# Optimization experiments

Measured on AMD Instinct MI355X. Metric: run time of the kernel, lower is better.

Reference implementation:

```python
import jax, jax.numpy as jnp
import numpy as np
from jax import lax

IMG = 512            # image H = W
FH = FW = 32         # feature map spatial size
A = 9                # anchors per location (3 sizes x 3 ratios)
N = FH * FW * A      # total anchors = 9216
IOU_THR = 0.7
MIN_SCORE = 0.5
MIN_SIZE = 1e-3


def make_anchors():
    """Anchors in centroid format (cx, cy, w, h), ordered (H, W, A)."""
    stride = IMG / FH
    sizes = np.array([32.0, 64.0, 128.0])
    ratios = np.array([0.5, 1.0, 2.0])
    ws = (sizes[:, None] / np.sqrt(ratios)[None, :]).reshape(-1)  # (A,)
    hs = (sizes[:, None] * np.sqrt(ratios)[None, :]).reshape(-1)  # (A,)
    cx = (np.arange(FW) + 0.5) * stride
    cy = (np.arange(FH) + 0.5) * stride
    CX = np.broadcast_to(cx[None, :, None], (FH, FW, A))
    CY = np.broadcast_to(cy[:, None, None], (FH, FW, A))
    Wg = np.broadcast_to(ws[None, None, :], (FH, FW, A))
    Hg = np.broadcast_to(hs[None, None, :], (FH, FW, A))
    anc = np.stack([CX, CY, Wg, Hg], axis=-1).reshape(-1, 4)
    return jnp.asarray(anc, dtype=jnp.float32)


def pairwise_iou(b):
    # b: (N,4) corners x1,y1,x2,y2
    x1, y1, x2, y2 = b[:, 0], b[:, 1], b[:, 2], b[:, 3]
    area = (x2 - x1) * (y2 - y1)
    ix1 = jnp.maximum(x1[:, None], x1[None, :])
    iy1 = jnp.maximum(y1[:, None], y1[None, :])
    ix2 = jnp.minimum(x2[:, None], x2[None, :])
    iy2 = jnp.minimum(y2[:, None], y2[None, :])
    inter = jnp.maximum(ix2 - ix1, 0.0) * jnp.maximum(iy2 - iy1, 0.0)
    union = area[:, None] + area[None, :] - inter
    return inter / jnp.maximum(union, 1e-9)


def nms_keep(boxes, scores, valid):
    """Greedy NMS. Returns bool keep mask of shape (N,). Index decisions only."""
    s = jnp.where(valid, scores, -jnp.inf)
    order = jnp.argsort(-s)
    b = boxes[order]
    v = valid[order]
    ious = pairwise_iou(b)  # (N, N)
    idx = jnp.arange(N)

    def body(i, supp):
        keep_i = (~supp[i]) & v[i]
        return supp | (keep_i & (ious[i] > IOU_THR) & (idx > i))

    supp = lax.fori_loop(0, N, body, jnp.zeros(N, dtype=bool))
    keep_sorted = (~supp) & v
    return jnp.zeros(N, dtype=bool).at[order].set(keep_sorted)


def setup_inputs() -> dict:
    key = jax.random.key(0)
    ks = jax.random.split(key, 4)
    return {
        "feature_map": jax.random.normal(ks[0], (1, 256, FH, FW), jnp.float32),
        "conv1_w": jax.random.normal(ks[1], (512, 256, 3, 3), jnp.float32) * 0.02,
        "conv1_b": jnp.zeros((512,), jnp.float32),
        "conv2_w": jax.random.normal(ks[2], (A, 512), jnp.float32) * 0.01,
        "conv2_b": jnp.zeros((A,), jnp.float32),
        "conv3_w": jax.random.normal(ks[3], (4 * A, 512), jnp.float32) * 0.01,
        "conv3_b": jnp.zeros((4 * A,), jnp.float32),
    }


def reference(feature_map, conv1_w, conv1_b, conv2_w, conv2_b, conv3_w, conv3_b):
    anchors = make_anchors()  # (N,4) cx,cy,w,h

    # --- conv backbone head ---
    h = lax.conv_general_dilated(
        feature_map, conv1_w, (1, 1), "SAME",
        dimension_numbers=("NCHW", "OIHW", "NCHW"))
    h = jax.nn.relu(h + conv1_b[None, :, None, None])  # (1,512,H,W)

    scores = jax.nn.sigmoid(
        jnp.einsum("bchw,ac->bahw", h, conv2_w) + conv2_b[None, :, None, None])
    scores = scores.transpose(0, 2, 3, 1).reshape(-1)  # (N,) ordered (H,W,A)

    off = jnp.einsum("bchw,oc->bohw", h, conv3_w) + conv3_b[None, :, None, None]
    off = off.reshape(1, A, 4, FH, FW).transpose(0, 3, 4, 1, 2).reshape(-1, 4)

    acx, acy, aw, ah = anchors[:, 0], anchors[:, 1], anchors[:, 2], anchors[:, 3]
    cx = acx + off[:, 0] * aw
    cy = acy + off[:, 1] * ah
    bw = aw * jnp.exp(off[:, 2])
    bh = ah * jnp.exp(off[:, 3])
    boxes = jnp.stack([cx - bw / 2, cy - bh / 2, cx + bw / 2, cy + bh / 2], axis=1)

    # --- clip to image ---
    lo = jnp.array([0.0, 0.0, 0.0, 0.0], jnp.float32)
    hi = jnp.array([IMG, IMG, IMG, IMG], jnp.float32)
    boxes = jnp.clip(boxes, lo, hi)

    # --- remove small boxes + score threshold (as a mask, jit-safe) ---
    valid = ((boxes[:, 2] - boxes[:, 0]) >= MIN_SIZE) \
          & ((boxes[:, 3] - boxes[:, 1]) >= MIN_SIZE) \
          & (scores >= MIN_SCORE)

    # --- NMS (selection is index-based; no gradient through the decision) ---
    keep = nms_keep(lax.stop_gradient(boxes), lax.stop_gradient(scores), valid)

    out = jnp.concatenate(
        [boxes * keep[:, None].astype(boxes.dtype),
         (scores * keep.astype(scores.dtype))[:, None]], axis=1)  # (N,5)
    return out
```

## Files before the change

### kernel.cpp

```cpp
#include <hip/hip_runtime.h>
#include <math.h>

#define FHW   32
#define NA    9
#define NBOX  9216
#define C1    256
#define C2    512
#define KTOT  2304
#define KS    8
#define KCH   (KTOT / KS)
#define BK    16
#define NT    (KCH / BK)
#define CAP   64
#define CAPL  4

struct AnchorWH { float w[NA]; float h[NA]; };

#define FP_OFF    0u
#define WT_OFF    1183744u
#define HP_OFF    5902336u
#define BOX_OFF   22679552u
#define SC_OFF    22827008u
#define VL_OFF    22863872u
#define DEG_OFF   22900736u
#define ADJ_OFF   22937600u
#define NV_OFF    24117248u

__global__ __launch_bounds__(256) void k_prep(const float* __restrict__ fin,
                                              float* __restrict__ Fp,
                                              unsigned int* __restrict__ deg,
                                              unsigned int* __restrict__ nv,
                                              const float* __restrict__ w1,
                                              float* __restrict__ Wt,
                                              float* __restrict__ out) {
    if (blockIdx.x < 1156) {
        int idx = blockIdx.x * 256 + threadIdx.x;
        if (idx < 256 * 34 * 34) {
            int c   = idx / 1156;
            int rem = idx - c * 1156;
            int yy  = rem / 34;
            int xx  = rem - yy * 34;
            float v = 0.f;
            if (yy >= 1 && yy <= 32 && xx >= 1 && xx <= 32)
                v = fin[c * 1024 + (yy - 1) * 32 + (xx - 1)];
            Fp[idx] = v;
        }
        if (idx < NBOX)     deg[idx] = 0u;
        if (idx < NBOX * 5) out[idx] = 0.f;
        if (idx == 0)       *nv = 0u;
    } else {
        __shared__ float tile[32][33];
        int tb  = blockIdx.x - 1156;
        int k0  = (tb % 72) * 32;
        int oc0 = (tb / 72) * 32;
        int t   = threadIdx.x;
        int r0 = t >> 5, c = t & 31;
        #pragma unroll
        for (int i = 0; i < 4; ++i) {
            int r = r0 + 8 * i;
            tile[r][c] = w1[(oc0 + r) * KTOT + k0 + c];
        }
        __syncthreads();
        #pragma unroll
        for (int i = 0; i < 4; ++i) {
            int kk  = r0 + 8 * i;
            int k   = k0 + kk;
            int ch  = k / 9;
            int kap = k - ch * 9;
            Wt[(kap * 256 + ch) * C2 + oc0 + c] = tile[c][kk];
        }
    }
}

__global__ __launch_bounds__(256) void k_gemm(const float* __restrict__ Fp,
                                              const float* __restrict__ Wt,
                                              float* __restrict__ hp) {
    const int id = blockIdx.x;
    const int kz = id & 7;
    const int g  = id >> 3;
    const int by = g & 3, bx = g >> 2;
    const int p0  = bx * 128;
    const int oc0 = by * 128;
    const int k0b = kz * KCH;
    const int t  = threadIdx.x;
    const int ty = t >> 4, tx = t & 15;

    __shared__ float As[BK][128];
    __shared__ float Bs[BK][128];

    const int pp  = t & 127;
    const int th  = t >> 7;
    const int pyx = ((p0 + pp) >> 5) * 34 + ((p0 + pp) & 31);
    const int rB  = t >> 5;
    const int cB  = (t & 31) * 4;

    float acc[2][2][4][4];
    #pragma unroll
    for (int rh = 0; rh < 2; ++rh)
        #pragma unroll
        for (int ch = 0; ch < 2; ++ch)
            #pragma unroll
            for (int r = 0; r < 4; ++r)
                #pragma unroll
                for (int c = 0; c < 4; ++c) acc[rh][ch][r][c] = 0.f;

    float  aS[8];
    float4 bS0, bS1;

    auto LOAD = [&](int s) {
        int tap = s >> 8, c0 = s & 255;
        int dy  = (tap * 11) >> 5;
        int dx  = tap - 3 * dy;
        const float* ab = Fp + ((c0 + th) * 34 + dy) * 34 + dx + pyx;
        #pragma unroll
        for (int i = 0; i < 8; ++i) aS[i] = ab[i * 2312];
        const float* bb = Wt + (s + rB) * C2 + oc0 + cB;
        bS0 = *(const float4*)bb;
        bS1 = *(const float4*)(bb + 8 * C2);
    };
    auto STORE = [&]() {
        #pragma unroll
        for (int i = 0; i < 8; ++i) As[2 * i + th][pp] = aS[i];
        *(float4*)&Bs[rB][cB]     = bS0;
        *(float4*)&Bs[rB + 8][cB] = bS1;
    };

    LOAD(k0b);
    #pragma unroll 1
    for (int tile = 0; tile < NT; ++tile) {
        __syncthreads();
        STORE();
        __syncthreads();
        if (tile + 1 < NT) LOAD(k0b + (tile + 1) * BK);
        #pragma unroll
        for (int kk = 0; kk < BK; ++kk) {
            float a[2][4], b[2][4];
            *(float4*)&a[0][0] = *(const float4*)&As[kk][ty * 4];
            *(float4*)&a[1][0] = *(const float4*)&As[kk][ty * 4 + 64];
            *(float4*)&b[0][0] = *(const float4*)&Bs[kk][tx * 4];
            *(float4*)&b[1][0] = *(const float4*)&Bs[kk][tx * 4 + 64];
            #pragma unroll
            for (int rh = 0; rh < 2; ++rh)
                #pragma unroll
                for (int ch = 0; ch < 2; ++ch)
                    #pragma unroll
                    for (int r = 0; r < 4; ++r)
                        #pragma unroll
                        for (int c = 0; c < 4; ++c)
                            acc[rh][ch][r][c] = fmaf(a[rh][r], b[ch][c], acc[rh][ch][r][c]);
        }
    }

    #pragma unroll
    for (int rh = 0; rh < 2; ++rh)
        #pragma unroll
        for (int r = 0; r < 4; ++r) {
            int p = p0 + rh * 64 + ty * 4 + r;
            float* dst = hp + ((size_t)(kz * 1024 + p)) * C2 + oc0 + tx * 4;
            *(float4*)dst        = *(float4*)&acc[rh][0][r][0];
            *(float4*)(dst + 64) = *(float4*)&acc[rh][1][r][0];
        }
}

__global__ __launch_bounds__(256) void k_heads(const float* __restrict__ hp,
                                               const float* __restrict__ b1,
                                               const float* __restrict__ w2,
                                               const float* __restrict__ b2,
                                               const float* __restrict__ w3,
                                               const float* __restrict__ b3,
                                               float* __restrict__ boxes,
                                               float* __restrict__ scoresG,
                                               unsigned int* __restrict__ nv,
                                               unsigned int* __restrict__ vlist,
                                               AnchorWH awh) {
    const int p0 = blockIdx.x * 4;
    const int t  = threadIdx.x;
    __shared__ float hrow[4][C2];
    __shared__ float arr[4][45];

    #pragma unroll
    for (int px = 0; px < 4; ++px) {
        int p = p0 + px;
        #pragma unroll
        for (int i = 0; i < 2; ++i) {
            int c = t + 256 * i;
            float s = b1[c];
            #pragma unroll
            for (int ks = 0; ks < KS; ++ks) s += hp[((size_t)(ks * 1024 + p)) * C2 + c];
            hrow[px][c] = fmaxf(s, 0.f);
        }
    }
    __syncthreads();

    const int w = t >> 6, lane = t & 63;
    for (int job = w; job < 180; job += 4) {
        int px = job / 45, j = job - px * 45;
        const float* wp = (j < 9) ? (w2 + j * C2) : (w3 + (j - 9) * C2);
        float s = 0.f;
        #pragma unroll
        for (int i = 0; i < 8; ++i) s += hrow[px][lane + 64 * i] * wp[lane + 64 * i];
        #pragma unroll
        for (int d = 1; d < 64; d <<= 1) s += __shfl_xor(s, d, 64);
        if (lane == 0) arr[px][j] = s;
    }
    __syncthreads();

    if (t < 36) {
        int px = t / 9, a = t - px * 9;
        int p = p0 + px;
        float logit = arr[px][a] + b2[a];
        float score = 1.f / (1.f + expf(-logit));
        float o0 = arr[px][9 + a * 4 + 0] + b3[a * 4 + 0];
        float o1 = arr[px][9 + a * 4 + 1] + b3[a * 4 + 1];
        float o2 = arr[px][9 + a * 4 + 2] + b3[a * 4 + 2];
        float o3 = arr[px][9 + a * 4 + 3] + b3[a * 4 + 3];
        int y = p >> 5, x = p & 31;
        float ax = (x + 0.5f) * 16.f, ay = (y + 0.5f) * 16.f;
        float aw = awh.w[a], ah = awh.h[a];
        float cx = ax + o0 * aw;
        float cy = ay + o1 * ah;
        float bw = aw * expf(o2);
        float bh = ah * expf(o3);
        float x1 = fminf(fmaxf(cx - bw * 0.5f, 0.f), 512.f);
        float y1 = fminf(fmaxf(cy - bh * 0.5f, 0.f), 512.f);
        float x2 = fminf(fmaxf(cx + bw * 0.5f, 0.f), 512.f);
        float y2 = fminf(fmaxf(cy + bh * 0.5f, 0.f), 512.f);
        int n = p * 9 + a;
        float4 bx4; bx4.x = x1; bx4.y = y1; bx4.z = x2; bx4.w = y2;
        ((float4*)boxes)[n] = bx4;
        scoresG[n] = score;
        bool valid = (x2 - x1 >= 0.001f) && (y2 - y1 >= 0.001f) && (score >= 0.5f);
        if (valid) {
            unsigned int ci = atomicAdd(nv, 1u);
            vlist[ci] = (unsigned int)n;
        }
    }
}

__global__ __launch_bounds__(256) void k_adj(const unsigned int* __restrict__ nvp,
                                             const unsigned int* __restrict__ vlist,
                                             const float* __restrict__ boxes,
                                             const float* __restrict__ scoresG,
                                             unsigned int* __restrict__ deg,
                                             unsigned short* __restrict__ adj) {
    const int Nv = (int)*nvp;
    int b = blockIdx.x;
    int tv = (int)(sqrtf(2.f * b + 0.25f) - 0.5f);
    while ((tv + 1) * (tv + 2) / 2 <= b) tv++;
    while (tv * (tv + 1) / 2 > b) tv--;
    int tu = b - tv * (tv + 1) / 2;
    if (tv * 128 >= Nv) return;

    __shared__ float4 ub[128], vb[128];
    __shared__ float  us[128], vs[128];
    __shared__ int    uo[128], vo[128];
    int t = threadIdx.x;
    if (t < 128) {
        int gi = tu * 128 + t;
        if (gi < Nv) { int n = (int)vlist[gi]; ub[t] = ((const float4*)boxes)[n]; us[t] = scoresG[n]; uo[t] = n; }
        else us[t] = -1.f;
    } else {
        int tt = t - 128;
        int gj = tv * 128 + tt;
        if (gj < Nv) { int n = (int)vlist[gj]; vb[tt] = ((const float4*)boxes)[n]; vs[tt] = scoresG[n]; vo[tt] = n; }
        else vs[tt] = -1.f;
    }
    __syncthreads();

    for (int s = 0; s < 64; ++s) {
        int q  = t + 256 * s;
        int i  = q >> 7, jj = q & 127;
        if (tu == tv && i >= jj) continue;
        float su = us[i], sv = vs[jj];
        if (su < 0.f || sv < 0.f) continue;
        float4 bu = ub[i], bv = vb[jj];
        float au = (bu.z - bu.x) * (bu.w - bu.y);
        float av = (bv.z - bv.x) * (bv.w - bv.y);
        float ix1 = fmaxf(bu.x, bv.x), iy1 = fmaxf(bu.y, bv.y);
        float ix2 = fminf(bu.z, bv.z), iy2 = fminf(bu.w, bv.w);
        float inter = fmaxf(ix2 - ix1, 0.f) * fmaxf(iy2 - iy1, 0.f);
        float uni = au + av - inter;
        float iou = inter / fmaxf(uni, 1e-9f);
        if (iou > 0.7f) {
            int gi = tu * 128 + i, gj = tv * 128 + jj;
            bool uHigh = (su > sv) || (su == sv && uo[i] < vo[jj]);
            int hi = uHigh ? gi : gj;
            int lo = uHigh ? gj : gi;
            unsigned int old = atomicAdd(&deg[hi], 1u);
            if ((old & 0xFFFFu) < CAP) {
                adj[hi * CAP + (old & 0xFFFFu)] = (unsigned short)lo;
                atomicAdd(&deg[lo], 0x10000u);
            }
        }
    }
}

__global__ __launch_bounds__(512) void k_peel(const unsigned int* __restrict__ nvp,
                                              const unsigned int* __restrict__ vlist,
                                              const unsigned int* __restrict__ degG,
                                              const unsigned short* __restrict__ adjG,
                                              const float* __restrict__ boxes,
                                              const float* __restrict__ scoresG,
                                              float* __restrict__ out) {
    __shared__ unsigned int   word[NBOX];
    __shared__ unsigned char  st[NBOX];
    __shared__ unsigned short outL[NBOX * CAPL];
    const int t  = threadIdx.x;
    const int Nv = (int)*nvp;
    const int chunk = (Nv + 511) / 512;
    const int i0 = t * chunk;
    const int i1 = (i0 + chunk < Nv) ? (i0 + chunk) : Nv;

    unsigned int amask = 0, smask = 0;
    for (int i = i0; i < i1; ++i) {
        unsigned int dg = degG[i];
        int cin  = (int)(dg >> 16);
        int dout = (int)(dg & 0xFFFFu); if (dout > CAP) dout = CAP;
        int dl = (dout < CAPL) ? dout : CAPL;
        for (int s = 0; s < dl; ++s)
            outL[i * CAPL + s] = adjG[i * CAP + s];
        word[i] = (unsigned int)cin;
        st[i] = 0;
        if (cin == 0) smask |= 1u << (i - i0);
        else          amask |= 1u << (i - i0);
    }
    __syncthreads();

    auto PUSH = [&](int i, bool kept) {
        unsigned int dg = degG[i];
        int dout = (int)(dg & 0xFFFFu); if (dout > CAP) dout = CAP;
        unsigned int delta = kept ? 0xFFFFu : 0xFFFFFFFFu;
        for (int s = 0; s < dout; ++s) {
            int j = (s < CAPL) ? (int)outL[i * CAPL + s]
                               : (int)adjG[i * CAP + s];
            atomicAdd(&word[j], delta);
        }
    };

    {
        unsigned int m = smask;
        while (m) {
            int b = __ffs(m) - 1; m &= m - 1;
            int i = i0 + b;
            st[i] = 1;
            PUSH(i, true);
        }
    }

    {
        volatile unsigned int* vw = word;
        int idle = 0;
        while (__any(amask != 0u)) {
            bool prog = false;
            unsigned int m = amask;
            while (m) {
                int b = __ffs(m) - 1; m &= m - 1;
                int i = i0 + b;
                unsigned int w = vw[i];
                if ((w & 0xFFFFu) == 0u) {
                    bool kept = (w >> 16) == 0u;
                    st[i] = kept ? 1 : 2;
                    PUSH(i, kept);
                    amask &= ~(1u << b);
                    prog = true;
                }
            }
            if (__any(prog)) idle = 0;
            else {
                if (++idle > 8000) break;
                __builtin_amdgcn_s_sleep(1);
            }
        }
    }
    __syncthreads();

    for (int i = i0; i < i1; ++i) {
        if (st[i] == 1) {
            int n = (int)vlist[i];
            float4 b = ((const float4*)boxes)[n];
            out[n * 5 + 0] = b.x;
            out[n * 5 + 1] = b.y;
            out[n * 5 + 2] = b.z;
            out[n * 5 + 3] = b.w;
            out[n * 5 + 4] = scoresG[n];
        }
    }
}

extern "C" void kernel_launch(void* const* d_in, const int* in_sizes, int n_in,
                              void* d_out, int out_size, void* d_ws, size_t ws_size,
                              hipStream_t stream) {
    const float* fin = (const float*)d_in[0];
    const float* w1  = (const float*)d_in[1];
    const float* b1  = (const float*)d_in[2];
    const float* w2  = (const float*)d_in[3];
    const float* b2  = (const float*)d_in[4];
    const float* w3  = (const float*)d_in[5];
    const float* b3  = (const float*)d_in[6];
    float* out = (float*)d_out;

    char* ws = (char*)d_ws;
    float*          Fp    = (float*)(ws + FP_OFF);
    float*          Wt    = (float*)(ws + WT_OFF);
    float*          hp    = (float*)(ws + HP_OFF);
    float*          boxes = (float*)(ws + BOX_OFF);
    float*          sc    = (float*)(ws + SC_OFF);
    unsigned int*   vlist = (unsigned int*)(ws + VL_OFF);
    unsigned int*   deg   = (unsigned int*)(ws + DEG_OFF);
    unsigned short* adj   = (unsigned short*)(ws + ADJ_OFF);
    unsigned int*   nv    = (unsigned int*)(ws + NV_OFF);

    AnchorWH awh;
    {
        const double sizes[3]  = {32.0, 64.0, 128.0};
        const double ratios[3] = {0.5, 1.0, 2.0};
        for (int si = 0; si < 3; ++si)
            for (int ri = 0; ri < 3; ++ri) {
                awh.w[si * 3 + ri] = (float)(sizes[si] / sqrt(ratios[ri]));
                awh.h[si * 3 + ri] = (float)(sizes[si] * sqrt(ratios[ri]));
            }
    }

    k_prep<<<dim3(1156 + 72 * 16), 256, 0, stream>>>(fin, Fp, deg, nv, w1, Wt, out);
    k_gemm<<<dim3(256), 256, 0, stream>>>(Fp, Wt, hp);
    k_heads<<<dim3(256), 256, 0, stream>>>(hp, b1, w2, b2, w3, b3, boxes, sc, nv, vlist, awh);
    k_adj<<<dim3(72 * 73 / 2), 256, 0, stream>>>(nv, vlist, boxes, sc, deg, adj);
    k_peel<<<dim3(1), 512, 0, stream>>>(nv, vlist, deg, adj, boxes, sc, out);
}
```

Measured before the change: 194.0 us.

## Double-buffer GEMM shared reads, persistent-grid adjacency kernel, cache out-degree in peel

```diff
diff --git a/kernel.cpp b/kernel.cpp
--- a/kernel.cpp
+++ b/kernel.cpp
@@ -125,6 +125,27 @@
         *(float4*)&Bs[rB + 8][cB] = bS1;
     };
 
+    float a0[2][4], b0[2][4], a1[2][4], b1[2][4];
+    auto LDA = [&](float (&d)[2][4], int kk) {
+        *(float4*)&d[0][0] = *(const float4*)&As[kk][ty * 4];
+        *(float4*)&d[1][0] = *(const float4*)&As[kk][ty * 4 + 64];
+    };
+    auto LDB = [&](float (&d)[2][4], int kk) {
+        *(float4*)&d[0][0] = *(const float4*)&Bs[kk][tx * 4];
+        *(float4*)&d[1][0] = *(const float4*)&Bs[kk][tx * 4 + 64];
+    };
+    auto FMA = [&](const float (&a)[2][4], const float (&b)[2][4]) {
+        #pragma unroll
+        for (int rh = 0; rh < 2; ++rh)
+            #pragma unroll
+            for (int ch = 0; ch < 2; ++ch)
+                #pragma unroll
+                for (int r = 0; r < 4; ++r)
+                    #pragma unroll
+                    for (int c = 0; c < 4; ++c)
+                        acc[rh][ch][r][c] = fmaf(a[rh][r], b[ch][c], acc[rh][ch][r][c]);
+    };
+
     LOAD(k0b);
     #pragma unroll 1
     for (int tile = 0; tile < NT; ++tile) {
@@ -132,22 +153,13 @@
         STORE();
         __syncthreads();
         if (tile + 1 < NT) LOAD(k0b + (tile + 1) * BK);
-        #pragma unroll
-        for (int kk = 0; kk < BK; ++kk) {
-            float a[2][4], b[2][4];
-            *(float4*)&a[0][0] = *(const float4*)&As[kk][ty * 4];
-            *(float4*)&a[1][0] = *(const float4*)&As[kk][ty * 4 + 64];
-            *(float4*)&b[0][0] = *(const float4*)&Bs[kk][tx * 4];
-            *(float4*)&b[1][0] = *(const float4*)&Bs[kk][tx * 4 + 64];
-            #pragma unroll
-            for (int rh = 0; rh < 2; ++rh)
-                #pragma unroll
-                for (int ch = 0; ch < 2; ++ch)
-                    #pragma unroll
-                    for (int r = 0; r < 4; ++r)
-                        #pragma unroll
-                        for (int c = 0; c < 4; ++c)
-                            acc[rh][ch][r][c] = fmaf(a[rh][r], b[ch][c], acc[rh][ch][r][c]);
+        LDA(a0, 0); LDB(b0, 0);
+        #pragma unroll
+        for (int kk = 0; kk < BK; kk += 2) {
+            LDA(a1, kk + 1); LDB(b1, kk + 1);
+            FMA(a0, b0);
+            if (kk + 2 < BK) { LDA(a0, kk + 2); LDB(b0, kk + 2); }
+            FMA(a1, b1);
         }
     }
 
@@ -244,54 +256,59 @@
                                              unsigned int* __restrict__ deg,
                                              unsigned short* __restrict__ adj) {
     const int Nv = (int)*nvp;
-    int b = blockIdx.x;
-    int tv = (int)(sqrtf(2.f * b + 0.25f) - 0.5f);
-    while ((tv + 1) * (tv + 2) / 2 <= b) tv++;
-    while (tv * (tv + 1) / 2 > b) tv--;
-    int tu = b - tv * (tv + 1) / 2;
-    if (tv * 128 >= Nv) return;
+    const int T  = (Nv + 127) >> 7;
+    const int NP = T * (T + 1) / 2;
+    int t = threadIdx.x;
 
     __shared__ float4 ub[128], vb[128];
     __shared__ float  us[128], vs[128];
     __shared__ int    uo[128], vo[128];
-    int t = threadIdx.x;
-    if (t < 128) {
-        int gi = tu * 128 + t;
-        if (gi < Nv) { int n = (int)vlist[gi]; ub[t] = ((const float4*)boxes)[n]; us[t] = scoresG[n]; uo[t] = n; }
-        else us[t] = -1.f;
-    } else {
-        int tt = t - 128;
-        int gj = tv * 128 + tt;
-        if (gj < Nv) { int n = (int)vlist[gj]; vb[tt] = ((const float4*)boxes)[n]; vs[tt] = scoresG[n]; vo[tt] = n; }
-        else vs[tt] = -1.f;
-    }
-    __syncthreads();
-
-    for (int s = 0; s < 64; ++s) {
-        int q  = t + 256 * s;
-        int i  = q >> 7, jj = q & 127;
-        if (tu == tv && i >= jj) continue;
-        float su = us[i], sv = vs[jj];
-        if (su < 0.f || sv < 0.f) continue;
-        float4 bu = ub[i], bv = vb[jj];
-        float au = (bu.z - bu.x) * (bu.w - bu.y);
-        float av = (bv.z - bv.x) * (bv.w - bv.y);
-        float ix1 = fmaxf(bu.x, bv.x), iy1 = fmaxf(bu.y, bv.y);
-        float ix2 = fminf(bu.z, bv.z), iy2 = fminf(bu.w, bv.w);
-        float inter = fmaxf(ix2 - ix1, 0.f) * fmaxf(iy2 - iy1, 0.f);
-        float uni = au + av - inter;
-        float iou = inter / fmaxf(uni, 1e-9f);
-        if (iou > 0.7f) {
-            int gi = tu * 128 + i, gj = tv * 128 + jj;
-            bool uHigh = (su > sv) || (su == sv && uo[i] < vo[jj]);
-            int hi = uHigh ? gi : gj;
-            int lo = uHigh ? gj : gi;
-            unsigned int old = atomicAdd(&deg[hi], 1u);
-            if ((old & 0xFFFFu) < CAP) {
-                adj[hi * CAP + (old & 0xFFFFu)] = (unsigned short)lo;
-                atomicAdd(&deg[lo], 0x10000u);
+
+    for (int b = blockIdx.x; b < NP; b += gridDim.x) {
+        int tv = (int)(sqrtf(2.f * b + 0.25f) - 0.5f);
+        while ((tv + 1) * (tv + 2) / 2 <= b) tv++;
+        while (tv * (tv + 1) / 2 > b) tv--;
+        int tu = b - tv * (tv + 1) / 2;
+
+        if (t < 128) {
+            int gi = tu * 128 + t;
+            if (gi < Nv) { int n = (int)vlist[gi]; ub[t] = ((const float4*)boxes)[n]; us[t] = scoresG[n]; uo[t] = n; }
+            else us[t] = -1.f;
+        } else {
+            int tt = t - 128;
+            int gj = tv * 128 + tt;
+            if (gj < Nv) { int n = (int)vlist[gj]; vb[tt] = ((const float4*)boxes)[n]; vs[tt] = scoresG[n]; vo[tt] = n; }
+            else vs[tt] = -1.f;
+        }
+        __syncthreads();
+
+        for (int s = 0; s < 64; ++s) {
+            int q  = t + 256 * s;
+            int i  = q >> 7, jj = q & 127;
+            if (tu == tv && i >= jj) continue;
+            float su = us[i], sv = vs[jj];
+            if (su < 0.f || sv < 0.f) continue;
+            float4 bu = ub[i], bv = vb[jj];
+            float au = (bu.z - bu.x) * (bu.w - bu.y);
+            float av = (bv.z - bv.x) * (bv.w - bv.y);
+            float ix1 = fmaxf(bu.x, bv.x), iy1 = fmaxf(bu.y, bv.y);
+            float ix2 = fminf(bu.z, bv.z), iy2 = fminf(bu.w, bv.w);
+            float inter = fmaxf(ix2 - ix1, 0.f) * fmaxf(iy2 - iy1, 0.f);
+            float uni = au + av - inter;
+            float iou = inter / fmaxf(uni, 1e-9f);
+            if (iou > 0.7f) {
+                int gi = tu * 128 + i, gj = tv * 128 + jj;
+                bool uHigh = (su > sv) || (su == sv && uo[i] < vo[jj]);
+                int hi = uHigh ? gi : gj;
+                int lo = uHigh ? gj : gi;
+                unsigned int old = atomicAdd(&deg[hi], 1u);
+                if ((old & 0xFFFFu) < CAP) {
+                    adj[hi * CAP + (old & 0xFFFFu)] = (unsigned short)lo;
+                    atomicAdd(&deg[lo], 0x10000u);
+                }
             }
         }
+        __syncthreads();
     }
 }
 
@@ -304,6 +321,7 @@
                                               float* __restrict__ out) {
     __shared__ unsigned int   word[NBOX];
     __shared__ unsigned char  st[NBOX];
+    __shared__ unsigned char  doutL[NBOX];
     __shared__ unsigned short outL[NBOX * CAPL];
     const int t  = threadIdx.x;
     const int Nv = (int)*nvp;
@@ -314,21 +332,21 @@
     unsigned int amask = 0, smask = 0;
     for (int i = i0; i < i1; ++i) {
         unsigned int dg = degG[i];
-        int cin  = (int)(dg >> 16);
+        unsigned int cin = dg >> 16;
         int dout = (int)(dg & 0xFFFFu); if (dout > CAP) dout = CAP;
+        doutL[i] = (unsigned char)dout;
         int dl = (dout < CAPL) ? dout : CAPL;
         for (int s = 0; s < dl; ++s)
             outL[i * CAPL + s] = adjG[i * CAP + s];
-        word[i] = (unsigned int)cin;
+        word[i] = cin;
         st[i] = 0;
-        if (cin == 0) smask |= 1u << (i - i0);
-        else          amask |= 1u << (i - i0);
+        if (cin == 0u) smask |= 1u << (i - i0);
+        else           amask |= 1u << (i - i0);
     }
     __syncthreads();
 
     auto PUSH = [&](int i, bool kept) {
-        unsigned int dg = degG[i];
-        int dout = (int)(dg & 0xFFFFu); if (dout > CAP) dout = CAP;
+        int dout = (int)doutL[i];
         unsigned int delta = kept ? 0xFFFFu : 0xFFFFFFFFu;
         for (int s = 0; s < dout; ++s) {
             int j = (s < CAPL) ? (int)outL[i * CAPL + s]
@@ -424,6 +442,6 @@
     k_prep<<<dim3(1156 + 72 * 16), 256, 0, stream>>>(fin, Fp, deg, nv, w1, Wt, out);
     k_gemm<<<dim3(256), 256, 0, stream>>>(Fp, Wt, hp);
     k_heads<<<dim3(256), 256, 0, stream>>>(hp, b1, w2, b2, w3, b3, boxes, sc, nv, vlist, awh);
-    k_adj<<<dim3(72 * 73 / 2), 256, 0, stream>>>(nv, vlist, boxes, sc, deg, adj);
+    k_adj<<<dim3(512), 256, 0, stream>>>(nv, vlist, boxes, sc, deg, adj);
     k_peel<<<dim3(1), 512, 0, stream>>>(nv, vlist, deg, adj, boxes, sc, out);
 }
```

After: 207.4 us. 6.9% more time.

## Raise GEMM split-K, vectorize heads reduction, persistent adjacency grid, cache peel degrees

Applied to the files above, without the earlier changes.

```diff
diff --git a/kernel.cpp b/kernel.cpp
--- a/kernel.cpp
+++ b/kernel.cpp
@@ -7,10 +7,7 @@
 #define C1    256
 #define C2    512
 #define KTOT  2304
-#define KS    8
-#define KCH   (KTOT / KS)
 #define BK    16
-#define NT    (KCH / BK)
 #define CAP   64
 #define CAPL  4
 
@@ -19,12 +16,6 @@
 #define FP_OFF    0u
 #define WT_OFF    1183744u
 #define HP_OFF    5902336u
-#define BOX_OFF   22679552u
-#define SC_OFF    22827008u
-#define VL_OFF    22863872u
-#define DEG_OFF   22900736u
-#define ADJ_OFF   22937600u
-#define NV_OFF    24117248u
 
 __global__ __launch_bounds__(256) void k_prep(const float* __restrict__ fin,
                                               float* __restrict__ Fp,
@@ -74,14 +65,18 @@
 
 __global__ __launch_bounds__(256) void k_gemm(const float* __restrict__ Fp,
                                               const float* __restrict__ Wt,
-                                              float* __restrict__ hp) {
+                                              float* __restrict__ hp,
+                                              int kshift) {
+    const int KCHd  = KTOT >> kshift;
+    const int NTd   = KCHd >> 4;
+    const int kmask = (1 << kshift) - 1;
     const int id = blockIdx.x;
-    const int kz = id & 7;
-    const int g  = id >> 3;
+    const int kz = id & kmask;
+    const int g  = id >> kshift;
     const int by = g & 3, bx = g >> 2;
     const int p0  = bx * 128;
     const int oc0 = by * 128;
-    const int k0b = kz * KCH;
+    const int k0b = kz * KCHd;
     const int t  = threadIdx.x;
     const int ty = t >> 4, tx = t & 15;
 
@@ -127,11 +122,11 @@
 
     LOAD(k0b);
     #pragma unroll 1
-    for (int tile = 0; tile < NT; ++tile) {
+    for (int tile = 0; tile < NTd; ++tile) {
         __syncthreads();
         STORE();
         __syncthreads();
-        if (tile + 1 < NT) LOAD(k0b + (tile + 1) * BK);
+        if (tile + 1 < NTd) LOAD(k0b + (tile + 1) * BK);
         #pragma unroll
         for (int kk = 0; kk < BK; ++kk) {
             float a[2][4], b[2][4];
@@ -172,36 +167,50 @@
                                                float* __restrict__ scoresG,
                                                unsigned int* __restrict__ nv,
                                                unsigned int* __restrict__ vlist,
-                                               AnchorWH awh) {
+                                               AnchorWH awh, int KSd) {
     const int p0 = blockIdx.x * 4;
     const int t  = threadIdx.x;
     __shared__ float hrow[4][C2];
     __shared__ float arr[4][45];
 
-    #pragma unroll
-    for (int px = 0; px < 4; ++px) {
-        int p = p0 + px;
-        #pragma unroll
-        for (int i = 0; i < 2; ++i) {
-            int c = t + 256 * i;
-            float s = b1[c];
-            #pragma unroll
-            for (int ks = 0; ks < KS; ++ks) s += hp[((size_t)(ks * 1024 + p)) * C2 + c];
-            hrow[px][c] = fmaxf(s, 0.f);
+    {
+        const int c4 = t & 127;
+        const int ph = t >> 7;
+        #pragma unroll
+        for (int px2 = 0; px2 < 2; ++px2) {
+            int px = px2 * 2 + ph;
+            int p  = p0 + px;
+            float4 s = ((const float4*)b1)[c4];
+            for (int ks = 0; ks < KSd; ++ks) {
+                float4 v = ((const float4*)hp)[(size_t)(ks * 1024 + p) * 128 + c4];
+                s.x += v.x; s.y += v.y; s.z += v.z; s.w += v.w;
+            }
+            s.x = fmaxf(s.x, 0.f); s.y = fmaxf(s.y, 0.f);
+            s.z = fmaxf(s.z, 0.f); s.w = fmaxf(s.w, 0.f);
+            *(float4*)&hrow[px][c4 * 4] = s;
         }
     }
     __syncthreads();
 
-    const int w = t >> 6, lane = t & 63;
-    for (int job = w; job < 180; job += 4) {
-        int px = job / 45, j = job - px * 45;
-        const float* wp = (j < 9) ? (w2 + j * C2) : (w3 + (j - 9) * C2);
-        float s = 0.f;
-        #pragma unroll
-        for (int i = 0; i < 8; ++i) s += hrow[px][lane + 64 * i] * wp[lane + 64 * i];
-        #pragma unroll
-        for (int d = 1; d < 64; d <<= 1) s += __shfl_xor(s, d, 64);
-        if (lane == 0) arr[px][j] = s;
+    {
+        const int grp = t >> 4, l = t & 15;
+        for (int r = 0; r < 12; ++r) {
+            int j180 = grp + (r << 4);
+            float s = 0.f;
+            int px = 0, j = 0;
+            if (j180 < 180) {
+                px = j180 / 45; j = j180 - px * 45;
+                const float* wp = (j < 9) ? (w2 + j * C2) : (w3 + (j - 9) * C2);
+                #pragma unroll
+                for (int i = 0; i < 32; ++i)
+                    s += hrow[px][l + 16 * i] * wp[l + 16 * i];
+            }
+            s += __shfl_xor(s, 1, 16);
+            s += __shfl_xor(s, 2, 16);
+            s += __shfl_xor(s, 4, 16);
+            s += __shfl_xor(s, 8, 16);
+            if (j180 < 180 && l == 0) arr[px][j] = s;
+        }
     }
     __syncthreads();
 
@@ -244,54 +253,59 @@
                                              unsigned int* __restrict__ deg,
                                              unsigned short* __restrict__ adj) {
     const int Nv = (int)*nvp;
-    int b = blockIdx.x;
-    int tv = (int)(sqrtf(2.f * b + 0.25f) - 0.5f);
-    while ((tv + 1) * (tv + 2) / 2 <= b) tv++;
-    while (tv * (tv + 1) / 2 > b) tv--;
-    int tu = b - tv * (tv + 1) / 2;
-    if (tv * 128 >= Nv) return;
+    const int T  = (Nv + 127) >> 7;
+    const int NP = T * (T + 1) / 2;
+    int t = threadIdx.x;
 
     __shared__ float4 ub[128], vb[128];
     __shared__ float  us[128], vs[128];
     __shared__ int    uo[128], vo[128];
-    int t = threadIdx.x;
-    if (t < 128) {
-        int gi = tu * 128 + t;
-        if (gi < Nv) { int n = (int)vlist[gi]; ub[t] = ((const float4*)boxes)[n]; us[t] = scoresG[n]; uo[t] = n; }
-        else us[t] = -1.f;
-    } else {
-        int tt = t - 128;
-        int gj = tv * 128 + tt;
-        if (gj < Nv) { int n = (int)vlist[gj]; vb[tt] = ((const float4*)boxes)[n]; vs[tt] = scoresG[n]; vo[tt] = n; }
-        else vs[tt] = -1.f;
-    }
-    __syncthreads();
-
-    for (int s = 0; s < 64; ++s) {
-        int q  = t + 256 * s;
-        int i  = q >> 7, jj = q & 127;
-        if (tu == tv && i >= jj) continue;
-        float su = us[i], sv = vs[jj];
-        if (su < 0.f || sv < 0.f) continue;
-        float4 bu = ub[i], bv = vb[jj];
-        float au = (bu.z - bu.x) * (bu.w - bu.y);
-        float av = (bv.z - bv.x) * (bv.w - bv.y);
-        float ix1 = fmaxf(bu.x, bv.x), iy1 = fmaxf(bu.y, bv.y);
-        float ix2 = fminf(bu.z, bv.z), iy2 = fminf(bu.w, bv.w);
-        float inter = fmaxf(ix2 - ix1, 0.f) * fmaxf(iy2 - iy1, 0.f);
-        float uni = au + av - inter;
-        float iou = inter / fmaxf(uni, 1e-9f);
-        if (iou > 0.7f) {
-            int gi = tu * 128 + i, gj = tv * 128 + jj;
-            bool uHigh = (su > sv) || (su == sv && uo[i] < vo[jj]);
-            int hi = uHigh ? gi : gj;
-            int lo = uHigh ? gj : gi;
-            unsigned int old = atomicAdd(&deg[hi], 1u);
-            if ((old & 0xFFFFu) < CAP) {
-                adj[hi * CAP + (old & 0xFFFFu)] = (unsigned short)lo;
-                atomicAdd(&deg[lo], 0x10000u);
-            }
-        }
+
+    for (int b = blockIdx.x; b < NP; b += gridDim.x) {
+        int tv = (int)(sqrtf(2.f * b + 0.25f) - 0.5f);
+        while ((tv + 1) * (tv + 2) / 2 <= b) tv++;
+        while (tv * (tv + 1) / 2 > b) tv--;
+        int tu = b - tv * (tv + 1) / 2;
+
+        if (t < 128) {
+            int gi = tu * 128 + t;
+            if (gi < Nv) { int n = (int)vlist[gi]; ub[t] = ((const float4*)boxes)[n]; us[t] = scoresG[n]; uo[t] = n; }
+            else us[t] = -1.f;
+        } else {
+            int tt = t - 128;
+            int gj = tv * 128 + tt;
+            if (gj < Nv) { int n = (int)vlist[gj]; vb[tt] = ((const float4*)boxes)[n]; vs[tt] = scoresG[n]; vo[tt] = n; }
+            else vs[tt] = -1.f;
+        }
+        __syncthreads();
+
+        for (int s = 0; s < 64; ++s) {
+            int q  = t + 256 * s;
+            int i  = q >> 7, jj = q & 127;
+            if (tu == tv && i >= jj) continue;
+            float su = us[i], sv = vs[jj];
+            if (su < 0.f || sv < 0.f) continue;
+            float4 bu = ub[i], bv = vb[jj];
+            float au = (bu.z - bu.x) * (bu.w - bu.y);
+            float av = (bv.z - bv.x) * (bv.w - bv.y);
+            float ix1 = fmaxf(bu.x, bv.x), iy1 = fmaxf(bu.y, bv.y);
+            float ix2 = fminf(bu.z, bv.z), iy2 = fminf(bu.w, bv.w);
+            float inter = fmaxf(ix2 - ix1, 0.f) * fmaxf(iy2 - iy1, 0.f);
+            float uni = au + av - inter;
+            float iou = inter / fmaxf(uni, 1e-9f);
+            if (iou > 0.7f) {
+                int gi = tu * 128 + i, gj = tv * 128 + jj;
+                bool uHigh = (su > sv) || (su == sv && uo[i] < vo[jj]);
+                int hi = uHigh ? gi : gj;
+                int lo = uHigh ? gj : gi;
+                unsigned int old = atomicAdd(&deg[hi], 1u);
+                if ((old & 0xFFFFu) < CAP) {
+                    adj[hi * CAP + (old & 0xFFFFu)] = (unsigned short)lo;
+                    atomicAdd(&deg[lo], 0x10000u);
+                }
+            }
+        }
+        __syncthreads();
     }
 }
 
@@ -304,6 +318,7 @@
                                               float* __restrict__ out) {
     __shared__ unsigned int   word[NBOX];
     __shared__ unsigned char  st[NBOX];
+    __shared__ unsigned char  doutL[NBOX];
     __shared__ unsigned short outL[NBOX * CAPL];
     const int t  = threadIdx.x;
     const int Nv = (int)*nvp;
@@ -314,21 +329,21 @@
     unsigned int amask = 0, smask = 0;
     for (int i = i0; i < i1; ++i) {
         unsigned int dg = degG[i];
-        int cin  = (int)(dg >> 16);
+        unsigned int cin = dg >> 16;
         int dout = (int)(dg & 0xFFFFu); if (dout > CAP) dout = CAP;
+        doutL[i] = (unsigned char)dout;
         int dl = (dout < CAPL) ? dout : CAPL;
         for (int s = 0; s < dl; ++s)
             outL[i * CAPL + s] = adjG[i * CAP + s];
-        word[i] = (unsigned int)cin;
+        word[i] = cin;
         st[i] = 0;
-        if (cin == 0) smask |= 1u << (i - i0);
-        else          amask |= 1u << (i - i0);
+        if (cin == 0u) smask |= 1u << (i - i0);
+        else           amask |= 1u << (i - i0);
     }
     __syncthreads();
 
     auto PUSH = [&](int i, bool kept) {
-        unsigned int dg = degG[i];
-        int dout = (int)(dg & 0xFFFFu); if (dout > CAP) dout = CAP;
+        int dout = (int)doutL[i];
         unsigned int delta = kept ? 0xFFFFu : 0xFFFFFFFFu;
         for (int s = 0; s < dout; ++s) {
             int j = (s < CAPL) ? (int)outL[i * CAPL + s]
@@ -367,8 +382,9 @@
             }
             if (__any(prog)) idle = 0;
             else {
-                if (++idle > 8000) break;
-                __builtin_amdgcn_s_sleep(1);
+                ++idle;
+                if (idle > 8000) break;
+                if (idle > 2) __builtin_amdgcn_s_sleep(1);
             }
         }
     }
@@ -399,16 +415,23 @@
     const float* b3  = (const float*)d_in[6];
     float* out = (float*)d_out;
 
+    const size_t need16 = (size_t)HP_OFF + 33554432u
+                        + 147456u + 3u * 36864u + 1179648u + 256u;
+    int kshift = (ws_size >= need16) ? 4 : 3;
+    int KSd = 1 << kshift;
+    size_t hpB = (size_t)KSd * 1024 * C2 * 4;
+
     char* ws = (char*)d_ws;
     float*          Fp    = (float*)(ws + FP_OFF);
     float*          Wt    = (float*)(ws + WT_OFF);
     float*          hp    = (float*)(ws + HP_OFF);
-    float*          boxes = (float*)(ws + BOX_OFF);
-    float*          sc    = (float*)(ws + SC_OFF);
-    unsigned int*   vlist = (unsigned int*)(ws + VL_OFF);
-    unsigned int*   deg   = (unsigned int*)(ws + DEG_OFF);
-    unsigned short* adj   = (unsigned short*)(ws + ADJ_OFF);
-    unsigned int*   nv    = (unsigned int*)(ws + NV_OFF);
+    size_t o = HP_OFF + hpB;
+    float*          boxes = (float*)(ws + o); o += (size_t)NBOX * 16;
+    float*          sc    = (float*)(ws + o); o += (size_t)NBOX * 4;
+    unsigned int*   vlist = (unsigned int*)(ws + o); o += (size_t)NBOX * 4;
+    unsigned int*   deg   = (unsigned int*)(ws + o); o += (size_t)NBOX * 4;
+    unsigned short* adj   = (unsigned short*)(ws + o); o += (size_t)NBOX * CAP * 2;
+    unsigned int*   nv    = (unsigned int*)(ws + o);
 
     AnchorWH awh;
     {
@@ -422,8 +445,8 @@
     }
 
     k_prep<<<dim3(1156 + 72 * 16), 256, 0, stream>>>(fin, Fp, deg, nv, w1, Wt, out);
-    k_gemm<<<dim3(256), 256, 0, stream>>>(Fp, Wt, hp);
-    k_heads<<<dim3(256), 256, 0, stream>>>(hp, b1, w2, b2, w3, b3, boxes, sc, nv, vlist, awh);
-    k_adj<<<dim3(72 * 73 / 2), 256, 0, stream>>>(nv, vlist, boxes, sc, deg, adj);
+    k_gemm<<<dim3(32 * KSd), 256, 0, stream>>>(Fp, Wt, hp, kshift);
+    k_heads<<<dim3(256), 256, 0, stream>>>(hp, b1, w2, b2, w3, b3, boxes, sc, nv, vlist, awh, KSd);
+    k_adj<<<dim3(512), 256, 0, stream>>>(nv, vlist, boxes, sc, deg, adj);
     k_peel<<<dim3(1), 512, 0, stream>>>(nv, vlist, deg, adj, boxes, sc, out);
 }
```

Measured after the change: 189.4 us. 1.02x faster.
